# Kernel tuning notes

Measured on AMD Instinct MI355X. Metric: run time of the kernel, lower is better.

Reference implementation:

```python
import jax, jax.numpy as jnp
import numpy as np

B, L, DIM = 2, 2048, 2048
NH, NKV, HD, WIN = 16, 8, 128, 128
N_REP = NH // NKV


def setup_inputs() -> dict:
    key = jax.random.key(0)
    ks = jax.random.split(key, 7)
    x = jax.random.normal(ks[0], (B, L, DIM), dtype=jnp.float32)
    cos = jax.random.uniform(ks[1], (L, HD), dtype=jnp.float32, minval=-1.0, maxval=1.0)
    sin = jax.random.uniform(ks[2], (L, HD), dtype=jnp.float32, minval=-1.0, maxval=1.0)
    s = 0.02
    wq = jax.random.normal(ks[3], (NH * HD, DIM), dtype=jnp.float32) * s
    wk = jax.random.normal(ks[4], (NKV * HD, DIM), dtype=jnp.float32) * s
    wv = jax.random.normal(ks[5], (NKV * HD, DIM), dtype=jnp.float32) * s
    wo = jax.random.normal(ks[6], (DIM, NH * HD), dtype=jnp.float32) * s
    return {"x": x, "cos": cos, "sin": sin, "wq": wq, "wk": wk, "wv": wv, "wo": wo}


def _rotate_half(t):
    t1, t2 = jnp.split(t, 2, axis=-1)
    return jnp.concatenate([-t2, t1], axis=-1)


def reference(x, cos, sin, wq, wk, wv, wo):
    # Projections (torch Linear: y = x @ W.T)
    q = (x @ wq.T).reshape(B, L, NH, HD).transpose(0, 2, 1, 3)    # (B, NH, L, HD)
    k = (x @ wk.T).reshape(B, L, NKV, HD).transpose(0, 2, 1, 3)   # (B, NKV, L, HD)
    v = (x @ wv.T).reshape(B, L, NKV, HD).transpose(0, 2, 1, 3)
    # RoPE (HF rotate_half convention), cos/sin broadcast over (B, heads)
    c = cos[None, None]  # (1,1,L,HD)
    s = sin[None, None]
    q = q * c + _rotate_half(q) * s
    k = k * c + _rotate_half(k) * s
    # GQA: repeat kv heads
    k = jnp.repeat(k, N_REP, axis=1)  # (B, NH, L, HD)
    v = jnp.repeat(v, N_REP, axis=1)
    scale = HD ** (-0.5)
    attn = jnp.einsum('bhqd,bhkd->bhqk', q, k) * scale  # (B, NH, L, L)
    rows = jnp.arange(L)[:, None]
    cols = jnp.arange(L)[None, :]
    combined_mask = (cols > rows) | (rows - cols > WIN)  # causal | out-of-window
    attn = jnp.where(combined_mask[None, None], -jnp.inf, attn)
    attn = jax.nn.softmax(attn, axis=-1)
    attn = jnp.nan_to_num(attn, nan=0.0)
    out = jnp.einsum('bhqk,bhkd->bhqd', attn, v)  # (B, NH, L, HD)
    out = out.transpose(0, 2, 1, 3).reshape(B, L, NH * HD)
    return out @ wo.T
```

## Files before the change

kernel.cpp:

```cpp
#include <hip/hip_runtime.h>
#include <stdint.h>

#define NB 2
#define NL 2048
#define NDIM 2048
#define NH 16
#define NKV 8
#define HD 128

typedef unsigned short u16;
typedef unsigned int u32;
using f32x4 = __attribute__((ext_vector_type(4))) float;
using bf16x8 = __attribute__((ext_vector_type(8))) short;

__device__ __forceinline__ u16 f2bf(float f){
  union { float f; u32 u; } v; v.f = f;
  u32 r = v.u + 0x7fffu + ((v.u >> 16) & 1u);
  return (u16)(r >> 16);
}
__device__ __forceinline__ float bf2f(u16 u){
  union { u32 u; float f; } v; v.u = ((u32)u) << 16;
  return v.f;
}

__device__ __forceinline__ void gld_lds16(const void* g, void* l){
  __builtin_amdgcn_global_load_lds(
      (const __attribute__((address_space(1))) u32*)g,
      (__attribute__((address_space(3))) u32*)l, 16, 0, 0);
}

#define X4   (NB*NL*NDIM/4)
#define WQ4  (NH*HD*NDIM/4)
#define WK4  (NKV*HD*NDIM/4)
#define WV4  (NKV*HD*NDIM/4)
#define WO4  (NDIM*NH*HD/4)
#define TOT4 (X4+WQ4+WK4+WV4+WO4)

__global__ __launch_bounds__(256) void cast_all(const float* __restrict__ x,
    const float* __restrict__ wq, const float* __restrict__ wk,
    const float* __restrict__ wv, const float* __restrict__ wo,
    u16* __restrict__ dst)
{
  int i = blockIdx.x * blockDim.x + threadIdx.x;
  int stride = gridDim.x * blockDim.x;
  for (; i < TOT4; i += stride){
    const float* src; int off;
    if      (i < X4)                 { src = x;  off = i; }
    else if (i < X4+WQ4)             { src = wq; off = i - X4; }
    else if (i < X4+WQ4+WK4)         { src = wk; off = i - (X4+WQ4); }
    else if (i < X4+WQ4+WK4+WV4)     { src = wv; off = i - (X4+WQ4+WK4); }
    else                             { src = wo; off = i - (X4+WQ4+WK4+WV4); }
    float4 f = ((const float4*)src)[off];
    ushort4 o;
    o.x = f2bf(f.x); o.y = f2bf(f.y); o.z = f2bf(f.z); o.w = f2bf(f.w);
    ((ushort4*)dst)[i] = o;
  }
}

template<int MODE>
__global__ __launch_bounds__(512, 2) void gemm8p(const u16* __restrict__ A,
    const u16* __restrict__ Bw, void* __restrict__ Cp, u16* __restrict__ ko,
    u16* __restrict__ vo, int M, int N, int K)
{
  extern __shared__ char lds[];
  const int tid = threadIdx.x;
  const int l = tid & 63, w = tid >> 6;
  const int wm = w >> 2, wn = w & 3;
  const int r = l & 15, cq = l >> 4;
  const int m0 = blockIdx.y << 8, n0 = blockIdx.x << 8;
  const int T = K >> 6;

  const int laneOff = (r * 64 + cq * 16) ^ ((r & 8) << 2);

  int stL[4];
  const u16* gA[4]; const u16* gB[4];
#pragma unroll
  for (int h = 0; h < 2; ++h)
#pragma unroll
    for (int g = 0; g < 2; ++g){
      int idx = h * 2 + g;
      int L = h * 16384 + (g * 512 + tid) * 16;
      int s  = L >> 10;
      int rr = (L >> 6) & 15;
      int c2 = (L & 63) ^ ((rr & 8) << 2);
      int row = ((s >> 1) << 4) | rr;
      int col = ((s & 1) << 5) | (c2 >> 1);
      stL[idx] = L;
      gA[idx] = A  + (size_t)(m0 + row) * K + col;
      gB[idx] = Bw + (size_t)(n0 + row) * K + col;
    }

#define ISSUE_A(h, v) do { if ((v) < T){ int _b = ((v) & 1) << 16;            \
    gld_lds16(gA[(h)*2+0] + (v)*64, lds + _b + stL[(h)*2+0]);                 \
    gld_lds16(gA[(h)*2+1] + (v)*64, lds + _b + stL[(h)*2+1]); } } while(0)
#define ISSUE_B(h, v) do { if ((v) < T){ int _b = (((v) & 1) << 16) + 32768;  \
    gld_lds16(gB[(h)*2+0] + (v)*64, lds + _b + stL[(h)*2+0]);                 \
    gld_lds16(gB[(h)*2+1] + (v)*64, lds + _b + stL[(h)*2+1]); } } while(0)

#define LDA(mi, kk) (*(const bf16x8*)(lds + bb + ((((wm*8+(mi))*2+(kk))) << 10) + laneOff))
#define LDB(ni, kk) (*(const bf16x8*)(lds + bb + 32768 + ((((wn*4+(ni))*2+(kk))) << 10) + laneOff))

#define BAR()    __builtin_amdgcn_s_barrier()
#define LGKM0()  do { asm volatile("s_waitcnt lgkmcnt(0)" ::: "memory"); \
                      __builtin_amdgcn_sched_barrier(0); } while(0)

  ISSUE_A(0, 0); ISSUE_A(1, 0);
  ISSUE_B(0, 0); ISSUE_B(1, 0);
  ISSUE_B(0, 1); ISSUE_B(1, 1);
  asm volatile("s_waitcnt vmcnt(4)" ::: "memory");
  BAR();

  f32x4 acc[8][4] = {};
  bf16x8 av[4][2], bv[4][2];

  for (int u = 0; u < T; ++u){
    const int bb = (u & 1) << 16;
#pragma unroll
    for (int mi = 0; mi < 4; ++mi){ av[mi][0] = LDA(mi, 0); av[mi][1] = LDA(mi, 1); }
#pragma unroll
    for (int ni = 0; ni < 2; ++ni){ bv[ni][0] = LDB(ni, 0); bv[ni][1] = LDB(ni, 1); }
    ISSUE_A(0, u + 1);
    BAR(); LGKM0();
    __builtin_amdgcn_s_setprio(1);
#pragma unroll
    for (int kk = 0; kk < 2; ++kk)
#pragma unroll
      for (int mi = 0; mi < 4; ++mi)
#pragma unroll
        for (int ni = 0; ni < 2; ++ni)
          acc[mi][ni] = __builtin_amdgcn_mfma_f32_16x16x32_bf16(av[mi][kk], bv[ni][kk], acc[mi][ni], 0, 0, 0);
    __builtin_amdgcn_s_setprio(0);
    BAR();
#pragma unroll
    for (int ni = 2; ni < 4; ++ni){ bv[ni][0] = LDB(ni, 0); bv[ni][1] = LDB(ni, 1); }
    ISSUE_A(1, u + 1);
    BAR(); LGKM0();
    __builtin_amdgcn_s_setprio(1);
#pragma unroll
    for (int kk = 0; kk < 2; ++kk)
#pragma unroll
      for (int mi = 0; mi < 4; ++mi)
#pragma unroll
        for (int ni = 2; ni < 4; ++ni)
          acc[mi][ni] = __builtin_amdgcn_mfma_f32_16x16x32_bf16(av[mi][kk], bv[ni][kk], acc[mi][ni], 0, 0, 0);
    __builtin_amdgcn_s_setprio(0);
    BAR();
#pragma unroll
    for (int mi = 0; mi < 4; ++mi){ av[mi][0] = LDA(mi + 4, 0); av[mi][1] = LDA(mi + 4, 1); }
    ISSUE_B(0, u + 2);
    BAR(); LGKM0();
    __builtin_amdgcn_s_setprio(1);
#pragma unroll
    for (int kk = 0; kk < 2; ++kk)
#pragma unroll
      for (int mi = 0; mi < 4; ++mi)
#pragma unroll
        for (int ni = 0; ni < 2; ++ni)
          acc[mi + 4][ni] = __builtin_amdgcn_mfma_f32_16x16x32_bf16(av[mi][kk], bv[ni][kk], acc[mi + 4][ni], 0, 0, 0);
    __builtin_amdgcn_s_setprio(0);
    BAR();
    ISSUE_B(1, u + 2);
    BAR(); LGKM0();
    __builtin_amdgcn_s_setprio(1);
#pragma unroll
    for (int kk = 0; kk < 2; ++kk)
#pragma unroll
      for (int mi = 0; mi < 4; ++mi)
#pragma unroll
        for (int ni = 2; ni < 4; ++ni)
          acc[mi + 4][ni] = __builtin_amdgcn_mfma_f32_16x16x32_bf16(av[mi][kk], bv[ni][kk], acc[mi + 4][ni], 0, 0, 0);
    __builtin_amdgcn_s_setprio(0);
    asm volatile("s_waitcnt vmcnt(4)" ::: "memory");
    BAR();
  }

#pragma unroll
  for (int mi = 0; mi < 8; ++mi)
#pragma unroll
    for (int ni = 0; ni < 4; ++ni){
      const int colg = n0 + wn * 64 + ni * 16 + r;
#pragma unroll
      for (int rg = 0; rg < 4; ++rg){
        const int row = m0 + wm * 128 + mi * 16 + cq * 4 + rg;
        if (MODE == 0){
          ((float*)Cp)[(size_t)row * N + colg] = acc[mi][ni][rg];
        } else {
          u16 val = f2bf(acc[mi][ni][rg]);
          if (colg < 2048)      ((u16*)Cp)[row * 2048 + colg] = val;
          else if (colg < 3072) ko[row * 1024 + (colg - 2048)] = val;
          else                  vo[row * 1024 + (colg - 3072)] = val;
        }
      }
    }
#undef ISSUE_A
#undef ISSUE_B
#undef LDA
#undef LDB
#undef BAR
#undef LGKM0
}

__global__ __launch_bounds__(256) void rope_kernel(u16* __restrict__ q, u16* __restrict__ k,
    const float* __restrict__ cosb, const float* __restrict__ sinb)
{
  const int row = blockIdx.x;
  const int pos = row & (NL - 1);
  const float* cr = cosb + pos * HD;
  const float* sr = sinb + pos * HD;
  const int t = threadIdx.x;
  {
    const int head = t >> 4;
    const int d0 = (t & 15) << 2;
    u16* base = q + row * (NH * HD) + head * HD + d0;
    ushort4 a = *(const ushort4*)base;
    ushort4 b = *(const ushort4*)(base + 64);
    float4 c1 = *(const float4*)(cr + d0);
    float4 s1 = *(const float4*)(sr + d0);
    float4 c2 = *(const float4*)(cr + 64 + d0);
    float4 s2 = *(const float4*)(sr + 64 + d0);
    ushort4 o1, o2;
    o1.x = f2bf(bf2f(a.x)*c1.x - bf2f(b.x)*s1.x);
    o1.y = f2bf(bf2f(a.y)*c1.y - bf2f(b.y)*s1.y);
    o1.z = f2bf(bf2f(a.z)*c1.z - bf2f(b.z)*s1.z);
    o1.w = f2bf(bf2f(a.w)*c1.w - bf2f(b.w)*s1.w);
    o2.x = f2bf(bf2f(b.x)*c2.x + bf2f(a.x)*s2.x);
    o2.y = f2bf(bf2f(b.y)*c2.y + bf2f(a.y)*s2.y);
    o2.z = f2bf(bf2f(b.z)*c2.z + bf2f(a.z)*s2.z);
    o2.w = f2bf(bf2f(b.w)*c2.w + bf2f(a.w)*s2.w);
    *(ushort4*)base = o1;
    *(ushort4*)(base + 64) = o2;
  }
  {
    const int head = t >> 5;
    const int d0 = (t & 31) << 1;
    u16* base = k + row * (NKV * HD) + head * HD + d0;
    ushort2 a = *(const ushort2*)base;
    ushort2 b = *(const ushort2*)(base + 64);
    float2 c1 = *(const float2*)(cr + d0);
    float2 s1 = *(const float2*)(sr + d0);
    float2 c2 = *(const float2*)(cr + 64 + d0);
    float2 s2 = *(const float2*)(sr + 64 + d0);
    ushort2 o1, o2;
    o1.x = f2bf(bf2f(a.x)*c1.x - bf2f(b.x)*s1.x);
    o1.y = f2bf(bf2f(a.y)*c1.y - bf2f(b.y)*s1.y);
    o2.x = f2bf(bf2f(b.x)*c2.x + bf2f(a.x)*s2.x);
    o2.y = f2bf(bf2f(b.y)*c2.y + bf2f(a.y)*s2.y);
    *(ushort2*)base = o1;
    *(ushort2*)(base + 64) = o2;
  }
}

__global__ __launch_bounds__(512) void attn_sw(const u16* __restrict__ q,
    const u16* __restrict__ k, const u16* __restrict__ v, u16* __restrict__ o)
{
  extern __shared__ u16 smem[];
  u16* kv0  = smem;
  u16* pbuf = smem + 2 * 16384;

  const int qb = blockIdx.x, h = blockIdx.y, b = blockIdx.z;
  const int kvh = h >> 1;
  const int tid = threadIdx.x, l = tid & 63, w = tid >> 6;
  const int lr = l & 15, lc = l >> 4;
  const int t0 = (qb == 0) ? 1 : 0;
  const int q0 = qb * 128;
  const int kst = NKV * HD;

#pragma unroll
  for (int t = 0; t < 2; ++t){
    if (t >= t0){
      const int kb = qb - 1 + t;
      const u16* kbase = k + (b * NL + kb * 128) * kst + kvh * HD;
#pragma unroll
      for (int c = 0; c < 4; ++c){
        int off = c * 8192 + tid * 16;
        int row = off >> 8;
        int ch  = (off >> 4) & 15;
        int gch = ch ^ (row & 7);
        gld_lds16(kbase + row * kst + gch * 8, kv0 + t * 16384 + (off >> 1));
      }
    }
  }

  bf16x8 aq[4];
  {
    const int qrow = b * NL + q0 + w * 16 + lr;
#pragma unroll
    for (int kc = 0; kc < 4; ++kc)
      aq[kc] = *(const bf16x8*)(q + qrow * (NH * HD) + h * HD + kc * 32 + lc * 8);
  }
  __syncthreads();

  f32x4 sc[2][8] = {};
  __builtin_amdgcn_s_setprio(1);
#pragma unroll
  for (int t = 0; t < 2; ++t){
#pragma unroll
    for (int cb = 0; cb < 8; ++cb){
      const bool live = (t == 0) ? (t0 == 0 && cb >= w) : (cb <= w);
      if (live){
        f32x4 a = {};
#pragma unroll
        for (int kc = 0; kc < 4; ++kc){
          int row = cb * 16 + lr;
          bf16x8 bk = *(const bf16x8*)(kv0 + t * 16384 +
              ((row * 256 + ((kc * 64 + lc * 16) ^ ((row & 7) << 4))) >> 1));
          a = __builtin_amdgcn_mfma_f32_16x16x32_bf16(aq[kc], bk, a, 0, 0, 0);
        }
        sc[t][cb] = a;
      }
    }
  }
  __builtin_amdgcn_s_setprio(0);

  const float scale = 0.08838834764831845f;
  float mx[4] = {-3e38f, -3e38f, -3e38f, -3e38f};
#pragma unroll
  for (int t = 0; t < 2; ++t)
#pragma unroll
    for (int cb = 0; cb < 8; ++cb){
      const bool liveF = (t == 0) ? (t0 == 0 && cb >= w) : (cb <= w);
      if (liveF){
#pragma unroll
        for (int r = 0; r < 4; ++r){
          int rbl = w * 16 + lc * 4 + r;
          int c = cb * 16 + lr;
          bool keep = (t == 0) ? (c >= rbl) : (c <= rbl);
          float val = keep ? sc[t][cb][r] * scale : -1e30f;
          sc[t][cb][r] = val;
          mx[r] = fmaxf(mx[r], val);
        }
      }
    }
#pragma unroll
  for (int r = 0; r < 4; ++r){
    mx[r] = fmaxf(mx[r], __shfl_xor(mx[r], 1));
    mx[r] = fmaxf(mx[r], __shfl_xor(mx[r], 2));
    mx[r] = fmaxf(mx[r], __shfl_xor(mx[r], 4));
    mx[r] = fmaxf(mx[r], __shfl_xor(mx[r], 8));
  }

  float sm[4] = {0.f, 0.f, 0.f, 0.f};
  u16* pw = pbuf + w * 4096;
#pragma unroll
  for (int t = 0; t < 2; ++t)
#pragma unroll
    for (int cb = 0; cb < 8; ++cb){
      const bool liveC = (t == 0) ? (t0 == 0 && cb >= w) : (cb <= w);
      const bool readN = (t == 0) ? (t0 == 0 && (cb | 1) >= w) : ((cb & ~1) <= w);
      if (liveC){
#pragma unroll
        for (int r = 0; r < 4; ++r){
          float p = __expf(sc[t][cb][r] - mx[r]);
          sm[r] += p;
          int rr = lc * 4 + r;
          int colb = (t * 128 + cb * 16 + lr) * 2;
          pw[((rr * 512 + colb) ^ ((rr & 7) << 4)) >> 1] = f2bf(p);
        }
      } else if (readN){
#pragma unroll
        for (int r = 0; r < 4; ++r){
          int rr = lc * 4 + r;
          int colb = (t * 128 + cb * 16 + lr) * 2;
          pw[((rr * 512 + colb) ^ ((rr & 7) << 4)) >> 1] = 0;
        }
      }
    }
#pragma unroll
  for (int r = 0; r < 4; ++r){
    sm[r] += __shfl_xor(sm[r], 1);
    sm[r] += __shfl_xor(sm[r], 2);
    sm[r] += __shfl_xor(sm[r], 4);
    sm[r] += __shfl_xor(sm[r], 8);
  }

  __syncthreads();

  {
    const int key = tid & 127;
    const int h2 = tid >> 7;
#pragma unroll
    for (int t = 0; t < 2; ++t){
      if (t >= t0){
        const int kb = qb - 1 + t;
        const u16* vbase = v + (b * NL + kb * 128 + key) * kst + kvh * HD + h2 * 32;
        u16* dst = kv0 + t * 16384;
#pragma unroll
        for (int c2 = 0; c2 < 4; ++c2){
          union { uint4 v4; u16 s[8]; } u;
          u.v4 = *(const uint4*)(vbase + c2 * 8);
          int d0 = h2 * 32 + c2 * 8;
#pragma unroll
          for (int e = 0; e < 8; ++e){
            int d = d0 + e;
            dst[((d * 256 + key * 2) ^ ((d & 7) << 4)) >> 1] = u.s[e];
          }
        }
      }
    }
  }
  __syncthreads();

  f32x4 od[8] = {};
  __builtin_amdgcn_s_setprio(1);
#pragma unroll
  for (int kc = 0; kc < 8; ++kc){
    const int t = kc >> 2, kl = kc & 3;
    const bool live = (t == 0) ? (t0 == 0 && (kl * 2 + 1) >= w) : (kl * 2 <= w);
    if (live){
      int abyte = ((lr * 512 + (kc * 32 + lc * 8) * 2) ^ ((lr & 7) << 4));
      bf16x8 pa = *(const bf16x8*)(pbuf + w * 4096 + (abyte >> 1));
#pragma unroll
      for (int cb = 0; cb < 8; ++cb){
        int d = cb * 16 + lr;
        bf16x8 vb = *(const bf16x8*)(kv0 + t * 16384 +
            ((d * 256 + ((kl * 64 + lc * 16) ^ ((d & 7) << 4))) >> 1));
        od[cb] = __builtin_amdgcn_mfma_f32_16x16x32_bf16(pa, vb, od[cb], 0, 0, 0);
      }
    }
  }
  __builtin_amdgcn_s_setprio(0);

  float inv[4];
#pragma unroll
  for (int r = 0; r < 4; ++r) inv[r] = 1.0f / sm[r];
#pragma unroll
  for (int cb = 0; cb < 8; ++cb)
#pragma unroll
    for (int r = 0; r < 4; ++r){
      int orow = b * NL + q0 + w * 16 + lc * 4 + r;
      int ocol = h * HD + cb * 16 + lr;
      o[orow * (NH * HD) + ocol] = f2bf(od[cb][r] * inv[r]);
    }
}

extern "C" void kernel_launch(void* const* d_in, const int* in_sizes, int n_in,
                              void* d_out, int out_size, void* d_ws, size_t ws_size,
                              hipStream_t stream)
{
  const float* x    = (const float*)d_in[0];
  const float* cosb = (const float*)d_in[1];
  const float* sinb = (const float*)d_in[2];
  const float* wq   = (const float*)d_in[3];
  const float* wk   = (const float*)d_in[4];
  const float* wv   = (const float*)d_in[5];
  const float* wo   = (const float*)d_in[6];

  u16* p = (u16*)d_ws;
  u16* xb   = p; p += NB * NL * NDIM;
  u16* wqkv = p; p += (NH + 2 * NKV) * HD * NDIM;
  u16* wob  = p; p += NDIM * NH * HD;
  u16* qb   = p; p += NB * NL * NH * HD;
  u16* kb   = p; p += NB * NL * NKV * HD;
  u16* vb   = p; p += NB * NL * NKV * HD;
  u16* ab   = p; p += NB * NL * NH * HD;

  cast_all<<<2048, 256, 0, stream>>>(x, wq, wk, wv, wo, xb);

  hipFuncSetAttribute(reinterpret_cast<const void*>(gemm8p<2>),
                      hipFuncAttributeMaxDynamicSharedMemorySize, 131072);
  hipFuncSetAttribute(reinterpret_cast<const void*>(gemm8p<0>),
                      hipFuncAttributeMaxDynamicSharedMemorySize, 131072);
  hipFuncSetAttribute(reinterpret_cast<const void*>(attn_sw),
                      hipFuncAttributeMaxDynamicSharedMemorySize, 131072);

  gemm8p<2><<<dim3(16, 16), 512, 131072, stream>>>(xb, wqkv, qb, kb, vb,
                                                   NB * NL, (NH + 2 * NKV) * HD, NDIM);

  rope_kernel<<<NB * NL, 256, 0, stream>>>(qb, kb, cosb, sinb);

  attn_sw<<<dim3(NL / 128, NH, NB), 512, 131072, stream>>>(qb, kb, vb, ab);

  gemm8p<0><<<dim3(8, 16), 512, 131072, stream>>>(ab, wob, d_out, nullptr, nullptr,
                                                  NB * NL, NDIM, NH * HD);
}
```

Before: 292.0 us.

## Add dedicated 128x256 Wo GEMM kernel and deepen QKV GEMM prefetch pipeline

The output projection now uses a new gemmWo kernel with a 128x256 tile, which doubles the grid to 256 blocks. It triple-buffers B and double-buffers A, issuing loads two iterations ahead. The QKV GEMM prefetch schedule is reorganised so more loads stay in flight (vmcnt 6), one barrier is removed, and the loop is unrolled by 2. The aim is to fill the GPU better for the small Wo GEMM and to hide global-to-LDS latency, at the cost of tricky buffer-reuse hazards and extra register use.

```diff
diff --git a/kernel.cpp b/kernel.cpp
--- a/kernel.cpp
+++ b/kernel.cpp
@@ -104,22 +104,22 @@
 #define LGKM0()  do { asm volatile("s_waitcnt lgkmcnt(0)" ::: "memory"); \
                       __builtin_amdgcn_sched_barrier(0); } while(0)
 
-  ISSUE_A(0, 0); ISSUE_A(1, 0);
-  ISSUE_B(0, 0); ISSUE_B(1, 0);
-  ISSUE_B(0, 1); ISSUE_B(1, 1);
-  asm volatile("s_waitcnt vmcnt(4)" ::: "memory");
+  ISSUE_A(0, 0); ISSUE_A(1, 0); ISSUE_B(0, 0); ISSUE_B(1, 0);
+  ISSUE_B(0, 1); ISSUE_A(0, 1); ISSUE_B(1, 1);
+  asm volatile("s_waitcnt vmcnt(6)" ::: "memory");
   BAR();
 
   f32x4 acc[8][4] = {};
   bf16x8 av[4][2], bv[4][2];
 
+#pragma unroll 2
   for (int u = 0; u < T; ++u){
     const int bb = (u & 1) << 16;
 #pragma unroll
     for (int mi = 0; mi < 4; ++mi){ av[mi][0] = LDA(mi, 0); av[mi][1] = LDA(mi, 1); }
 #pragma unroll
     for (int ni = 0; ni < 2; ++ni){ bv[ni][0] = LDB(ni, 0); bv[ni][1] = LDB(ni, 1); }
-    ISSUE_A(0, u + 1);
+    ISSUE_A(1, u + 1);
     BAR(); LGKM0();
     __builtin_amdgcn_s_setprio(1);
 #pragma unroll
@@ -133,7 +133,6 @@
     BAR();
 #pragma unroll
     for (int ni = 2; ni < 4; ++ni){ bv[ni][0] = LDB(ni, 0); bv[ni][1] = LDB(ni, 1); }
-    ISSUE_A(1, u + 1);
     BAR(); LGKM0();
     __builtin_amdgcn_s_setprio(1);
 #pragma unroll
@@ -159,8 +158,8 @@
           acc[mi + 4][ni] = __builtin_amdgcn_mfma_f32_16x16x32_bf16(av[mi][kk], bv[ni][kk], acc[mi + 4][ni], 0, 0, 0);
     __builtin_amdgcn_s_setprio(0);
     BAR();
+    ISSUE_A(0, u + 2);
     ISSUE_B(1, u + 2);
-    BAR(); LGKM0();
     __builtin_amdgcn_s_setprio(1);
 #pragma unroll
     for (int kk = 0; kk < 2; ++kk)
@@ -170,7 +169,8 @@
         for (int ni = 2; ni < 4; ++ni)
           acc[mi + 4][ni] = __builtin_amdgcn_mfma_f32_16x16x32_bf16(av[mi][kk], bv[ni][kk], acc[mi + 4][ni], 0, 0, 0);
     __builtin_amdgcn_s_setprio(0);
-    asm volatile("s_waitcnt vmcnt(4)" ::: "memory");
+    if (u + 2 < T) asm volatile("s_waitcnt vmcnt(6)" ::: "memory");
+    else           asm volatile("s_waitcnt vmcnt(0)" ::: "memory");
     BAR();
   }
 
@@ -196,8 +196,125 @@
 #undef ISSUE_B
 #undef LDA
 #undef LDB
-#undef BAR
-#undef LGKM0
+}
+
+__global__ __launch_bounds__(512, 2) void gemmWo(const u16* __restrict__ A,
+    const u16* __restrict__ Bw, float* __restrict__ Cp, int M, int N, int K)
+{
+  extern __shared__ char lds[];
+  const int tid = threadIdx.x;
+  const int l = tid & 63, w = tid >> 6;
+  const int wm = w >> 2, wn = w & 3;
+  const int r = l & 15, cq = l >> 4;
+  const int m0 = blockIdx.y << 7, n0 = blockIdx.x << 8;
+  const int T = K >> 6;
+
+  const int laneOff = (r * 64 + cq * 16) ^ ((r & 8) << 2);
+
+  int stg[2];
+  const u16* gWA[2]; const u16* gWB[4];
+#pragma unroll
+  for (int g = 0; g < 2; ++g){
+    stg[g] = (g * 512 + tid) * 16;
+    int L = stg[g];
+    int s  = L >> 10;
+    int rr = (L >> 6) & 15;
+    int c2 = (L & 63) ^ ((rr & 8) << 2);
+    int row = ((s >> 1) << 4) | rr;
+    int col = ((s & 1) << 5) | (c2 >> 1);
+    gWA[g] = A + (size_t)(m0 + row) * K + col;
+  }
+#pragma unroll
+  for (int h = 0; h < 2; ++h)
+#pragma unroll
+    for (int g = 0; g < 2; ++g){
+      int L = h * 16384 + stg[g];
+      int s  = L >> 10;
+      int rr = (L >> 6) & 15;
+      int c2 = (L & 63) ^ ((rr & 8) << 2);
+      int row = ((s >> 1) << 4) | rr;
+      int col = ((s & 1) << 5) | (c2 >> 1);
+      gWB[h * 2 + g] = Bw + (size_t)(n0 + row) * K + col;
+    }
+
+#define WISSUE_A(v, ab) do { if ((v) < T){ char* _d = lds + 98304 + (ab) * 16384; \
+    gld_lds16(gWA[0] + (v)*64, _d + stg[0]);                                      \
+    gld_lds16(gWA[1] + (v)*64, _d + stg[1]); } } while(0)
+#define WISSUE_B(h, v, b3) do { if ((v) < T){ char* _d = lds + (b3) * 32768 + (h) * 16384; \
+    gld_lds16(gWB[(h)*2+0] + (v)*64, _d + stg[0]);                                         \
+    gld_lds16(gWB[(h)*2+1] + (v)*64, _d + stg[1]); } } while(0)
+
+#define WLDA(mi, kk) (*(const bf16x8*)(lds + 98304 + curA * 16384 + ((((wm*4+(mi))*2+(kk))) << 10) + laneOff))
+#define WLDB(ni, kk) (*(const bf16x8*)(lds + curB * 32768 + ((((wn*4+(ni))*2+(kk))) << 10) + laneOff))
+
+  WISSUE_A(0, 0); WISSUE_B(0, 0, 0); WISSUE_B(1, 0, 0);
+  WISSUE_A(1, 1); WISSUE_B(0, 1, 1); WISSUE_B(1, 1, 1);
+  asm volatile("s_waitcnt vmcnt(6)" ::: "memory");
+  __builtin_amdgcn_s_barrier();
+
+  f32x4 acc[4][4] = {};
+  bf16x8 av[4][2], bv[4][2];
+  int c0 = 0;
+
+  for (int u = 0; u < T; ++u){
+    const int curA = u & 1;
+    const int curB = c0;
+    const int c2i = (c0 + 2 >= 3) ? (c0 - 1) : (c0 + 2);
+#pragma unroll
+    for (int mi = 0; mi < 4; ++mi){ av[mi][0] = WLDA(mi, 0); av[mi][1] = WLDA(mi, 1); }
+#pragma unroll
+    for (int ni = 0; ni < 2; ++ni){ bv[ni][0] = WLDB(ni, 0); bv[ni][1] = WLDB(ni, 1); }
+    __builtin_amdgcn_s_barrier();
+    asm volatile("s_waitcnt lgkmcnt(0)" ::: "memory");
+    __builtin_amdgcn_sched_barrier(0);
+    __builtin_amdgcn_s_setprio(1);
+#pragma unroll
+    for (int kk = 0; kk < 2; ++kk)
+#pragma unroll
+      for (int mi = 0; mi < 4; ++mi)
+#pragma unroll
+        for (int ni = 0; ni < 2; ++ni)
+          acc[mi][ni] = __builtin_amdgcn_mfma_f32_16x16x32_bf16(av[mi][kk], bv[ni][kk], acc[mi][ni], 0, 0, 0);
+    __builtin_amdgcn_s_setprio(0);
+    __builtin_amdgcn_s_barrier();
+#pragma unroll
+    for (int ni = 2; ni < 4; ++ni){ bv[ni][0] = WLDB(ni, 0); bv[ni][1] = WLDB(ni, 1); }
+    WISSUE_A(u + 2, curA);
+    WISSUE_B(0, u + 2, c2i);
+    WISSUE_B(1, u + 2, c2i);
+    __builtin_amdgcn_s_barrier();
+    asm volatile("s_waitcnt lgkmcnt(0)" ::: "memory");
+    __builtin_amdgcn_sched_barrier(0);
+    __builtin_amdgcn_s_setprio(1);
+#pragma unroll
+    for (int kk = 0; kk < 2; ++kk)
+#pragma unroll
+      for (int mi = 0; mi < 4; ++mi)
+#pragma unroll
+        for (int ni = 2; ni < 4; ++ni)
+          acc[mi][ni] = __builtin_amdgcn_mfma_f32_16x16x32_bf16(av[mi][kk], bv[ni][kk], acc[mi][ni], 0, 0, 0);
+    __builtin_amdgcn_s_setprio(0);
+    if (u + 2 < T) asm volatile("s_waitcnt vmcnt(6)" ::: "memory");
+    else           asm volatile("s_waitcnt vmcnt(0)" ::: "memory");
+    __builtin_amdgcn_s_barrier();
+    c0 = (c0 == 2) ? 0 : (c0 + 1);
+  }
+
+#pragma unroll
+  for (int mi = 0; mi < 4; ++mi)
+#pragma unroll
+    for (int ni = 0; ni < 4; ++ni){
+      const int colg = n0 + wn * 64 + ni * 16 + r;
+#pragma unroll
+      for (int rg = 0; rg < 4; ++rg){
+        const int row = m0 + wm * 64 + mi * 16 + cq * 4 + rg;
+        Cp[(size_t)row * N + colg] = acc[mi][ni][rg];
+      }
+    }
+#undef WISSUE_A
+#undef WISSUE_B
+#undef WLDA
+#undef WLDB
 }
 
 __global__ __launch_bounds__(256) void rope_kernel(u16* __restrict__ q, u16* __restrict__ k,
@@ -458,7 +575,7 @@
 
   hipFuncSetAttribute(reinterpret_cast<const void*>(gemm8p<2>),
                       hipFuncAttributeMaxDynamicSharedMemorySize, 131072);
-  hipFuncSetAttribute(reinterpret_cast<const void*>(gemm8p<0>),
+  hipFuncSetAttribute(reinterpret_cast<const void*>(gemmWo),
                       hipFuncAttributeMaxDynamicSharedMemorySize, 131072);
   hipFuncSetAttribute(reinterpret_cast<const void*>(attn_sw),
                       hipFuncAttributeMaxDynamicSharedMemorySize, 131072);
@@ -470,6 +587,6 @@
 
   attn_sw<<<dim3(NL / 128, NH, NB), 512, 131072, stream>>>(qb, kb, vb, ab);
 
-  gemm8p<0><<<dim3(8, 16), 512, 131072, stream>>>(ab, wob, d_out, nullptr, nullptr,
-                                                  NB * NL, NDIM, NH * HD);
-}
+  gemmWo<<<dim3(8, 32), 512, 131072, stream>>>(ab, wob, (float*)d_out,
+                                               NB * NL, NDIM, NH * HD);
+}
```

Result: faster. 278.0 us (-4.8%).
